# Performance work log

Measured on AMD Instinct MI355X. Metric: run time of the kernel, lower is better.

The kernel has to match this reference:

```python
import jax, jax.numpy as jnp
import numpy as np

C_DIM = 768
NH = 12
MLP_HIDDEN = 3072


def _ln(x, g, b, eps=1e-5):
    mu = x.mean(-1, keepdims=True)
    var = ((x - mu) ** 2).mean(-1, keepdims=True)
    return (x - mu) / jnp.sqrt(var + eps) * g + b


def _mha(x, Wqkv, nh, scale):
    # x: [N, L, C]; Wqkv: [C, 3C] packed as (3, nh, hd) on output dim
    N, L, C = x.shape
    hd = C // nh
    qkv = (x @ Wqkv).reshape(N, L, 3, nh, hd)
    q, k, v = qkv[:, :, 0], qkv[:, :, 1], qkv[:, :, 2]  # [N, L, nh, hd]
    a = jnp.einsum('nqhd,nkhd->nhqk', q, k) * scale
    a = jax.nn.softmax(a, axis=-1)
    o = jnp.einsum('nhqk,nkhd->nqhd', a, v).reshape(N, L, C)
    return o


def setup_inputs() -> dict:
    key = jax.random.key(0)
    ks = jax.random.split(key, 16)
    B, T, K, C = 4, 16, 196, C_DIM
    s = 0.02
    inp = {
        'x': jax.random.normal(ks[0], (B, 1 + K * T, C), jnp.float32),
        'B': B, 'T': T, 'K': K,
        'ln1_g': jnp.ones((C,)), 'ln1_b': jnp.zeros((C,)),
        'lnt_g': jnp.ones((C,)), 'lnt_b': jnp.zeros((C,)),
        'ln2_g': jnp.ones((C,)), 'ln2_b': jnp.zeros((C,)),
        'lncls_g': jnp.ones((C,)), 'lncls_b': jnp.zeros((C,)),
        'Wqkv_s': jax.random.normal(ks[1], (C, 3 * C)) * s,
        'Wproj_s': jax.random.normal(ks[2], (C, C)) * s,
        'bproj_s': jnp.zeros((C,)),
        'Wqkv4': jax.random.normal(ks[3], (C, 3 * C)) * s,
        'Wqkv8': jax.random.normal(ks[4], (C, 3 * C)) * s,
        'Wqkv16': jax.random.normal(ks[5], (C, 3 * C)) * s,
        'Wp4': jax.random.normal(ks[6], (C, C)) * s, 'bp4': jnp.zeros((C,)),
        'Wp8': jax.random.normal(ks[7], (C, C)) * s, 'bp8': jnp.zeros((C,)),
        'Wp16': jax.random.normal(ks[8], (C, C)) * s, 'bp16': jnp.zeros((C,)),
        'Wtfc': jax.random.normal(ks[9], (C, C)) * s, 'btfc': jnp.zeros((C,)),
        'Wfc1': jax.random.normal(ks[10], (C, MLP_HIDDEN)) * s, 'bfc1': jnp.zeros((MLP_HIDDEN,)),
        'Wfc2': jax.random.normal(ks[11], (MLP_HIDDEN, C)) * s, 'bfc2': jnp.zeros((C,)),
    }
    return inp


def reference(x, B, T, K, ln1_g, ln1_b, lnt_g, lnt_b, ln2_g, ln2_b,
              lncls_g, lncls_b, Wqkv_s, Wproj_s, bproj_s,
              Wqkv4, Wqkv8, Wqkv16, Wp4, bp4, Wp8, bp8, Wp16, bp16,
              Wtfc, btfc, Wfc1, bfc1, Wfc2, bfc2):
    C = x.shape[-1]
    nh = NH
    scale = (C // nh) ** -0.5
    t1, t2 = T // 4, T // 2

    # ---- multi-scale temporal attention (eval mode: all dropout identity) ----
    xt = x[:, 1:, :].reshape(B, K, T, C).reshape(B * K, T, C)
    xt_n = _ln(xt, lnt_g, lnt_b)
    x4 = _mha(xt_n[:, T - t1:], Wqkv4, nh, scale) @ Wp4 + bp4    # [BK, t1, C]
    x8 = _mha(xt_n[:, t2:], Wqkv8, nh, scale) @ Wp8 + bp8        # [BK, t2, C]
    x16 = _mha(xt_n, Wqkv16, nh, scale) @ Wp16 + bp16            # [BK, T, C]
    # windowed fusion of overlapping scales
    x8 = jnp.concatenate([x8[:, :t1], 0.5 * x8[:, t1:] + 0.5 * x4], axis=1)
    x16 = jnp.concatenate([x16[:, :t2], 0.5 * x16[:, t2:] + 0.5 * x8], axis=1)
    res_temp = x16.reshape(B, K * T, C)
    xt_full = res_temp @ Wtfc + btfc + x[:, 1:, :]               # [B, K*T, C]

    # ---- spatial attention with replicated CLS token ----
    init_cls = x[:, 0:1, :]                                      # [B, 1, C]
    cls_rep = jnp.broadcast_to(init_cls, (B, T, C)).reshape(B * T, 1, C)
    xs = xt_full.reshape(B, K, T, C).transpose(0, 2, 1, 3).reshape(B * T, K, C)
    xs = jnp.concatenate([cls_rep, xs], axis=1)                  # [B*T, K+1, C]
    res_spatial = _mha(_ln(xs, ln1_g, ln1_b), Wqkv_s, nh, scale) @ Wproj_s + bproj_s

    # ---- CLS aggregation over time ----
    cls_sp = _ln(res_spatial[:, 0, :].reshape(B, T, C), lncls_g, lncls_b)
    target = cls_sp[:, -1:, :]                                   # [B, 1, C]
    attn2 = jax.nn.softmax(jnp.einsum('bqc,btc->bqt', target, cls_sp), axis=-1)
    cls_sp = attn2 @ cls_sp                                      # [B, 1, C]

    x_s = res_spatial[:, 1:, :].reshape(B, T, K, C).transpose(0, 2, 1, 3).reshape(B, K * T, C)
    x_cat = jnp.concatenate([init_cls, xt_full], axis=1) + jnp.concatenate([cls_sp, x_s], axis=1)

    # ---- MLP residual ----
    h = _ln(x_cat, ln2_g, ln2_b)
    h = jax.nn.gelu(h @ Wfc1 + bfc1, approximate=False) @ Wfc2 + bfc2
    return x_cat + h
```

## Files before the change

### kernel.cpp

```cpp
#include <hip/hip_runtime.h>
#include <hip/hip_bf16.h>
#include <stdint.h>

#define BF16 __hip_bfloat16

typedef __attribute__((ext_vector_type(8))) short short8;
typedef __attribute__((ext_vector_type(2))) short short2v;
typedef __attribute__((ext_vector_type(4))) float floatx4;

typedef const __attribute__((address_space(1))) void* gas_cvp;
typedef __attribute__((address_space(3))) void* las_vp;

__device__ __forceinline__ float bf2f(BF16 v) { return __bfloat162float(v); }
__device__ __forceinline__ BF16 f2bf(float v) { return __float2bfloat16(v); }

__global__ __launch_bounds__(256) void wtrans(const float* __restrict__ W,
                                              BF16* __restrict__ Wt, int K, int N) {
    __shared__ float t[32][33];
    int k0 = blockIdx.x * 32, n0 = blockIdx.y * 32;
    int tx = threadIdx.x & 31, ty = threadIdx.x >> 5;
#pragma unroll
    for (int i = 0; i < 32; i += 8) t[ty + i][tx] = W[(size_t)(k0 + ty + i) * N + n0 + tx];
    __syncthreads();
#pragma unroll
    for (int i = 0; i < 32; i += 8)
        Wt[(size_t)(n0 + ty + i) * K + k0 + tx] = f2bf(t[tx][ty + i]);
}

struct WTJob { const float* src; BF16* dst; int K; int N; int boff; };
struct WTParams { WTJob j[12]; };

__global__ __launch_bounds__(256) void wtrans_all(WTParams P) {
    __shared__ float t[32][33];
    const int bid = blockIdx.x;
    int ji = 0;
#pragma unroll
    for (int i = 1; i < 12; ++i)
        if (bid >= P.j[i].boff) ji = i;
    const float* __restrict__ W = P.j[ji].src;
    BF16* __restrict__ Wt = P.j[ji].dst;
    const int K = P.j[ji].K, N = P.j[ji].N;
    const int lb = bid - P.j[ji].boff;
    const int kb = K >> 5;
    const int k0 = (lb % kb) * 32, n0 = (lb / kb) * 32;
    const int tx = threadIdx.x & 31, ty = threadIdx.x >> 5;
#pragma unroll
    for (int i = 0; i < 32; i += 8) t[ty + i][tx] = W[(size_t)(k0 + ty + i) * N + n0 + tx];
    __syncthreads();
#pragma unroll
    for (int i = 0; i < 32; i += 8)
        Wt[(size_t)(n0 + ty + i) * K + k0 + tx] = f2bf(t[tx][ty + i]);
}

template <int MODE>
__global__ __launch_bounds__(256) void ln_kernel(const float* __restrict__ src0,
                                                 const float* __restrict__ src1,
                                                 const BF16* __restrict__ srcb,
                                                 const float* __restrict__ g,
                                                 const float* __restrict__ bta,
                                                 BF16* __restrict__ dst_bf,
                                                 float* __restrict__ dst_f) {
    const int r = blockIdx.x, tid = threadIdx.x;
    float x0, x1, x2;
    {
        const float* src;
        if (MODE == 0) {
            int b = r / 3136, rr = r - b * 3136;
            src = src0 + ((size_t)b * 3137 + 1 + rr) * 768;
        } else if (MODE == 1) {
            int bt = r / 197, j = r - bt * 197;
            int b = bt >> 4, t = bt & 15;
            if (j == 0) src = src0 + (size_t)b * 3137 * 768;
            else        src = src1 + ((size_t)(b * 3137 + 1) + (size_t)(j - 1) * 16 + t) * 768;
        } else {
            src = src0 + (size_t)r * 768;
        }
        x0 = src[tid]; x1 = src[tid + 256]; x2 = src[tid + 512];
    }
    float s = x0 + x1 + x2;
    float ss = x0 * x0 + x1 * x1 + x2 * x2;
    __shared__ float red[8];
#pragma unroll
    for (int o = 32; o > 0; o >>= 1) { s += __shfl_down(s, o); ss += __shfl_down(ss, o); }
    if ((tid & 63) == 0) { red[tid >> 6] = s; red[4 + (tid >> 6)] = ss; }
    __syncthreads();
    s = red[0] + red[1] + red[2] + red[3];
    ss = red[4] + red[5] + red[6] + red[7];
    const float mu = s * (1.0f / 768.0f);
    const float var = ss * (1.0f / 768.0f) - mu * mu;
    const float rstd = rsqrtf(var + 1e-5f);
#pragma unroll
    for (int i = 0; i < 3; ++i) {
        int c = tid + i * 256;
        float xv = (i == 0) ? x0 : (i == 1) ? x1 : x2;
        float y = (xv - mu) * rstd * g[c] + bta[c];
        dst_bf[(size_t)r * 768 + c] = f2bf(y);
    }
}

template <int AMAP, int OMODE>
__device__ __forceinline__ void gemm_body(BF16* Al, BF16* Bl,
                                          int orig, int nwg, int gx,
                                          const BF16* __restrict__ A,
                                          const BF16* __restrict__ Bt,
                                          const float* __restrict__ bias,
                                          const void* res, void* Cout,
                                          int M, int N, int K) {
    const int tid = threadIdx.x;
    const int lane = tid & 63;
    const int w = tid >> 6;

    const int xcd = orig & 7;
    const int idx = orig >> 3;
    const int q8 = nwg >> 3, r8 = nwg & 7;
    const int wgid = (xcd < r8 ? xcd * (q8 + 1) : r8 * (q8 + 1) + (xcd - r8) * q8) + idx;
    const int bn0 = (wgid % gx) * 128;
    const int bm0 = (wgid / gx) * 128;

    const BF16* gsrc[8];
    BF16* ldst[8];
    const int rin = lane >> 3;
    const int kblk = (lane & 7) ^ rin;
#pragma unroll
    for (int j = 0; j < 8; ++j) {
        int c = w * 8 + j;
        if (c < 16) {
            int gr = bm0 + c * 8 + rin;
            if (gr > M - 1) gr = M - 1;
            if (AMAP == 1) gr = (gr >> 3) * 16 + 8 + (gr & 7);
            if (AMAP == 2) gr = (gr >> 2) * 16 + 12 + (gr & 3);
            gsrc[j] = A + (size_t)gr * K + kblk * 8;
            ldst[j] = Al + c * 512;
        } else {
            int gn = bn0 + (c - 16) * 8 + rin;
            gsrc[j] = Bt + (size_t)gn * K + kblk * 8;
            ldst[j] = Bl + (c - 16) * 512;
        }
    }

    const int wm = (w & 1) * 64;
    const int wn = (w >> 1) * 64;
    const int fr = lane & 15;
    const int fq = lane >> 4;
    const int sw = fr & 7;
    const int o0 = (fq ^ sw) * 8;
    const int o1 = ((fq + 4) ^ sw) * 8;
    const BF16* pa[4];
    const BF16* pb[4];
#pragma unroll
    for (int t = 0; t < 4; ++t) {
        pa[t] = Al + (wm + t * 16 + fr) * 64;
        pb[t] = Bl + (wn + t * 16 + fr) * 64;
    }

    floatx4 acc[4][4];
#pragma unroll
    for (int i = 0; i < 4; ++i)
#pragma unroll
        for (int j = 0; j < 4; ++j) acc[i][j] = (floatx4){0.f, 0.f, 0.f, 0.f};

    for (int k0 = 0; k0 < K; k0 += 64) {
#pragma unroll
        for (int j = 0; j < 8; ++j) {
            __builtin_amdgcn_global_load_lds((gas_cvp)gsrc[j], (las_vp)ldst[j], 16, 0, 0);
            gsrc[j] += 64;
        }
        __syncthreads();
        {
            short8 af[4], bfr[4];
#pragma unroll
            for (int t = 0; t < 4; ++t) {
                af[t] = *(const short8*)(pa[t] + o0);
                bfr[t] = *(const short8*)(pb[t] + o0);
            }
#pragma unroll
            for (int mt = 0; mt < 4; ++mt)
#pragma unroll
                for (int nt = 0; nt < 4; ++nt)
                    acc[mt][nt] = __builtin_amdgcn_mfma_f32_16x16x32_bf16(af[mt], bfr[nt], acc[mt][nt], 0, 0, 0);
#pragma unroll
            for (int t = 0; t < 4; ++t) {
                af[t] = *(const short8*)(pa[t] + o1);
                bfr[t] = *(const short8*)(pb[t] + o1);
            }
#pragma unroll
            for (int mt = 0; mt < 4; ++mt)
#pragma unroll
                for (int nt = 0; nt < 4; ++nt)
                    acc[mt][nt] = __builtin_amdgcn_mfma_f32_16x16x32_bf16(af[mt], bfr[nt], acc[mt][nt], 0, 0, 0);
        }
        __syncthreads();
    }

#pragma unroll
    for (int mt = 0; mt < 4; ++mt) {
#pragma unroll
        for (int nt = 0; nt < 4; ++nt) {
            const int gcol = bn0 + wn + nt * 16 + fr;
#pragma unroll
            for (int r = 0; r < 4; ++r) {
                const int grow = bm0 + wm + mt * 16 + fq * 4 + r;
                if (grow < M) {
                    float v = acc[mt][nt][r];
                    if (OMODE != 0 && OMODE != 8) v += bias[gcol];
                    if (OMODE == 0 || OMODE == 1) {
                        ((BF16*)Cout)[(size_t)grow * N + gcol] = f2bf(v);
                    } else if (OMODE == 2) {
                        int t8 = grow & 7;
                        int rr = (grow >> 3) * 16 + 8 + t8;
                        float w8 = (t8 < 4) ? 0.5f : 0.25f;
                        BF16* R = (BF16*)Cout;
                        size_t o = (size_t)rr * 768 + gcol;
                        R[o] = f2bf(0.5f * bf2f(R[o]) + w8 * v);
                    } else if (OMODE == 3) {
                        int t4 = grow & 3;
                        int rr = (grow >> 2) * 16 + 12 + t4;
                        BF16* R = (BF16*)Cout;
                        size_t o = (size_t)rr * 768 + gcol;
                        R[o] = f2bf(bf2f(R[o]) + 0.25f * v);
                    } else if (OMODE == 4) {
                        int b = grow / 3136;
                        size_t xrow = (size_t)b * 3137 + 1 + (grow - b * 3136);
                        ((float*)Cout)[xrow * 768 + gcol] =
                            v + ((const float*)res)[xrow * 768 + gcol];
                    } else if (OMODE == 6) {
                        float u = v * (0.7978845608f + 0.0356774081f * v * v);
                        v = v / (1.0f + __expf(-2.0f * u));
                        ((BF16*)Cout)[(size_t)grow * N + gcol] = f2bf(v);
                    } else {
                        v += ((const float*)res)[(size_t)grow * N + gcol];
                        ((float*)Cout)[(size_t)grow * N + gcol] = v;
                    }
                }
            }
        }
    }
}

template <int AMAP, int OMODE>
__global__ __launch_bounds__(256) void gemm_bf16(const BF16* __restrict__ A,
                                                 const BF16* __restrict__ Bt,
                                                 const float* __restrict__ bias,
                                                 const void* res,
                                                 void* Cout,
                                                 int M, int N, int K) {
    __shared__ BF16 Al[128 * 64];
    __shared__ BF16 Bl[128 * 64];
    const int gx = gridDim.x;
    const int nwg = gx * (int)gridDim.y;
    const int orig = (int)blockIdx.y * gx + (int)blockIdx.x;
    gemm_body<AMAP, OMODE>(Al, Bl, orig, nwg, gx, A, Bt, bias, res, Cout, M, N, K);
}

template <int AMAP0, int OMODE0, int AMAP1, int OMODE1>
__global__ __launch_bounds__(256) void gemm_dual(
        int nblk0, int gx0,
        const BF16* A0, const BF16* B0, const float* b0, const void* r0, void* C0,
        int M0, int N0, int K0,
        int gx1,
        const BF16* A1, const BF16* B1, const float* b1, const void* r1, void* C1,
        int M1, int N1, int K1) {
    __shared__ BF16 Al[128 * 64];
    __shared__ BF16 Bl[128 * 64];
    const int bid = blockIdx.x;
    if (bid < nblk0)
        gemm_body<AMAP0, OMODE0>(Al, Bl, bid, nblk0, gx0, A0, B0, b0, r0, C0, M0, N0, K0);
    else
        gemm_body<AMAP1, OMODE1>(Al, Bl, bid - nblk0, (int)gridDim.x - nblk0, gx1,
                                 A1, B1, b1, r1, C1, M1, N1, K1);
}

template <int L, int NT>
__global__ __launch_bounds__(NT) void temporal_attn(const BF16* __restrict__ qkv,
                                                    BF16* __restrict__ outp) {
    __shared__ float q[L * 64];
    __shared__ float k[L * 65];
    __shared__ float v[L * 64];
    __shared__ float S[L * L];
    const int bh = blockIdx.x;
    const int b = bh / 12, h = bh % 12;
    const int tid = threadIdx.x;
    const size_t rb = (size_t)b * L;
    for (int idx = tid; idx < L * 8; idx += NT) {
        int i = idx >> 3, d8 = (idx & 7) * 8;
        size_t base = (rb + i) * 2304 + h * 64 + d8;
        short8 qv = *(const short8*)(qkv + base);
        short8 kv = *(const short8*)(qkv + base + 768);
        short8 vv = *(const short8*)(qkv + base + 1536);
#pragma unroll
        for (int e = 0; e < 8; ++e) {
            q[i * 64 + d8 + e] = bf2f(((const BF16*)&qv)[e]);
            k[i * 65 + d8 + e] = bf2f(((const BF16*)&kv)[e]);
            v[i * 64 + d8 + e] = bf2f(((const BF16*)&vv)[e]);
        }
    }
    __syncthreads();
    for (int idx = tid; idx < L * L; idx += NT) {
        int i = idx / L, j = idx % L;
        float a = 0.f;
#pragma unroll
        for (int d = 0; d < 64; ++d) a += q[i * 64 + d] * k[j * 65 + d];
        S[idx] = a * 0.125f;
    }
    __syncthreads();
    if (tid < L) {
        float mx = -1e30f;
        for (int j = 0; j < L; ++j) mx = fmaxf(mx, S[tid * L + j]);
        float sm = 0.f;
        for (int j = 0; j < L; ++j) { float e = __expf(S[tid * L + j] - mx); S[tid * L + j] = e; sm += e; }
        float inv = 1.0f / sm;
        for (int j = 0; j < L; ++j) S[tid * L + j] *= inv;
    }
    __syncthreads();
    for (int idx = tid; idx < L * 8; idx += NT) {
        int i = idx >> 3, d8 = (idx & 7) * 8;
        float acc[8];
#pragma unroll
        for (int e = 0; e < 8; ++e) acc[e] = 0.f;
#pragma unroll
        for (int j = 0; j < L; ++j) {
            float sv = S[i * L + j];
#pragma unroll
            for (int e = 0; e < 8; ++e) acc[e] += sv * v[j * 64 + d8 + e];
        }
        short8 ov;
#pragma unroll
        for (int e = 0; e < 8; ++e) ((BF16*)&ov)[e] = f2bf(acc[e]);
        *(short8*)(outp + (rb + i) * 768 + h * 64 + d8) = ov;
    }
}

__global__ __launch_bounds__(256) void spatial_attn_mfma(const BF16* __restrict__ qkv,
                                                         BF16* __restrict__ outp) {
    const int bid = blockIdx.x;
    const int qt = bid & 3;
    const int h = (bid >> 2) % 12;
    const int bt = bid / 48;
    const int rowbase = bt * 197;
    __shared__ BF16 KsPl[208 * 72];
    __shared__ BF16 Vt[64 * 232];
    const int tid = threadIdx.x;
    const int lane = tid & 63;
    const int w = tid >> 6;
    const int ln = lane & 15;
    const int quad = lane >> 4;

    for (int it = tid; it < 208 * 8; it += 256) {
        int key = it >> 3, c = it & 7;
        int kc = key < 197 ? key : 196;
        short8 gk = *(const short8*)(qkv + (size_t)(rowbase + kc) * 2304 + 768 + h * 64 + c * 8);
        *(short8*)&KsPl[key * 72 + c * 8] = gk;
    }
    for (int it = tid; it < 112 * 8; it += 256) {
        int p = it >> 3, c = it & 7;
        int kc0 = (2 * p < 197) ? 2 * p : 196;
        int kc1 = (2 * p + 1 < 197) ? 2 * p + 1 : 196;
        short8 a = *(const short8*)(qkv + (size_t)(rowbase + kc0) * 2304 + 1536 + h * 64 + c * 8);
        short8 b = *(const short8*)(qkv + (size_t)(rowbase + kc1) * 2304 + 1536 + h * 64 + c * 8);
#pragma unroll
        for (int e = 0; e < 8; ++e) {
            short2v pr;
            pr[0] = a[e];
            pr[1] = b[e];
            *(short2v*)&Vt[(c * 8 + e) * 232 + 2 * p] = pr;
        }
    }
    __syncthreads();

    const int m0 = qt * 64 + w * 16;
    int qrow = m0 + ln; if (qrow > 196) qrow = 196;
    const BF16* qptr = qkv + (size_t)(rowbase + qrow) * 2304 + h * 64 + quad * 8;
    short8 aq0 = *(const short8*)(qptr);
    short8 aq1 = *(const short8*)(qptr + 32);

    floatx4 sacc[13];
#pragma unroll
    for (int nt = 0; nt < 13; ++nt) sacc[nt] = (floatx4){0.f, 0.f, 0.f, 0.f};
#pragma unroll
    for (int nt = 0; nt < 13; ++nt) {
        const BF16* kb = &KsPl[(nt * 16 + ln) * 72 + quad * 8];
        short8 b0 = *(const short8*)kb;
        short8 b1 = *(const short8*)(kb + 32);
        sacc[nt] = __builtin_amdgcn_mfma_f32_16x16x32_bf16(aq0, b0, sacc[nt], 0, 0, 0);
        sacc[nt] = __builtin_amdgcn_mfma_f32_16x16x32_bf16(aq1, b1, sacc[nt], 0, 0, 0);
    }
    __syncthreads();

#pragma unroll
    for (int r = 0; r < 4; ++r) {
        float mx = -1e30f;
#pragma unroll
        for (int nt = 0; nt < 13; ++nt) {
            float s = sacc[nt][r] * 0.125f;
            sacc[nt][r] = s;
            if (nt * 16 + ln < 197) mx = fmaxf(mx, s);
        }
        mx = fmaxf(mx, __shfl_xor(mx, 1));
        mx = fmaxf(mx, __shfl_xor(mx, 2));
        mx = fmaxf(mx, __shfl_xor(mx, 4));
        mx = fmaxf(mx, __shfl_xor(mx, 8));
        float sum = 0.f;
#pragma unroll
        for (int nt = 0; nt < 13; ++nt) {
            float e = (nt * 16 + ln < 197) ? __expf(sacc[nt][r] - mx) : 0.f;
            sacc[nt][r] = e;
            sum += e;
        }
        sum += __shfl_xor(sum, 1);
        sum += __shfl_xor(sum, 2);
        sum += __shfl_xor(sum, 4);
        sum += __shfl_xor(sum, 8);
        float inv = 1.0f / sum;
#pragma unroll
        for (int nt = 0; nt < 13; ++nt) sacc[nt][r] *= inv;
    }

    BF16* pw = KsPl + w * (16 * 232);
#pragma unroll
    for (int nt = 0; nt < 13; ++nt)
#pragma unroll
        for (int r = 0; r < 4; ++r)
            pw[(quad * 4 + r) * 232 + nt * 16 + ln] = f2bf(sacc[nt][r]);
#pragma unroll
    for (int r = 0; r < 4; ++r)
        pw[(quad * 4 + r) * 232 + 208 + ln] = f2bf(0.f);

    floatx4 oacc[4];
#pragma unroll
    for (int nt = 0; nt < 4; ++nt) oacc[nt] = (floatx4){0.f, 0.f, 0.f, 0.f};
    for (int kb = 0; kb < 7; ++kb) {
        short8 ap = *(const short8*)&pw[ln * 232 + kb * 32 + quad * 8];
#pragma unroll
        for (int nt = 0; nt < 4; ++nt) {
            short8 bv = *(const short8*)&Vt[(nt * 16 + ln) * 232 + kb * 32 + quad * 8];
            oacc[nt] = __builtin_amdgcn_mfma_f32_16x16x32_bf16(ap, bv, oacc[nt], 0, 0, 0);
        }
    }

#pragma unroll
    for (int nt = 0; nt < 4; ++nt) {
        int dim = nt * 16 + ln;
#pragma unroll
        for (int r = 0; r < 4; ++r) {
            int q = m0 + quad * 4 + r;
            if (q < 197)
                outp[(size_t)(rowbase + q) * 768 + h * 64 + dim] = f2bf(oacc[nt][r]);
        }
    }
}

__global__ __launch_bounds__(256) void cls_ln_attn_kernel(const BF16* __restrict__ res_sp,
                                                          const float* __restrict__ g,
                                                          const float* __restrict__ bta,
                                                          float* __restrict__ clsout) {
    const int b = blockIdx.x;
    const int tid = threadIdx.x;
    __shared__ float sLN[16][768];
    __shared__ float red[8];
    __shared__ float dots[16];
    __shared__ float aw[16];

    for (int t = 0; t < 16; ++t) {
        const BF16* src = res_sp + (size_t)((b * 16 + t) * 197) * 768;
        float x0 = bf2f(src[tid]);
        float x1 = bf2f(src[tid + 256]);
        float x2 = bf2f(src[tid + 512]);
        float s = x0 + x1 + x2;
        float ss = x0 * x0 + x1 * x1 + x2 * x2;
#pragma unroll
        for (int o = 32; o > 0; o >>= 1) { s += __shfl_down(s, o); ss += __shfl_down(ss, o); }
        if ((tid & 63) == 0) { red[tid >> 6] = s; red[4 + (tid >> 6)] = ss; }
        __syncthreads();
        s = red[0] + red[1] + red[2] + red[3];
        ss = red[4] + red[5] + red[6] + red[7];
        const float mu = s * (1.0f / 768.0f);
        const float var = ss * (1.0f / 768.0f) - mu * mu;
        const float rstd = rsqrtf(var + 1e-5f);
        sLN[t][tid]       = (x0 - mu) * rstd * g[tid] + bta[tid];
        sLN[t][tid + 256] = (x1 - mu) * rstd * g[tid + 256] + bta[tid + 256];
        sLN[t][tid + 512] = (x2 - mu) * rstd * g[tid + 512] + bta[tid + 512];
        __syncthreads();
    }

    const int t = tid >> 4, l16 = tid & 15;
    float p = 0.f;
    for (int c = l16; c < 768; c += 16) p += sLN[15][c] * sLN[t][c];
#pragma unroll
    for (int o = 8; o > 0; o >>= 1) p += __shfl_down(p, o, 16);
    if (l16 == 0) dots[t] = p;
    __syncthreads();
    if (tid == 0) {
        float mx = -1e30f;
        for (int j = 0; j < 16; ++j) mx = fmaxf(mx, dots[j]);
        float s = 0.f;
        for (int j = 0; j < 16; ++j) { aw[j] = __expf(dots[j] - mx); s += aw[j]; }
        float inv = 1.0f / s;
        for (int j = 0; j < 16; ++j) aw[j] *= inv;
    }
    __syncthreads();
    for (int c = tid; c < 768; c += 256) {
        float acc = 0.f;
#pragma unroll
        for (int j = 0; j < 16; ++j) acc += aw[j] * sLN[j][c];
        clsout[(size_t)b * 768 + c] = acc;
    }
}

__global__ __launch_bounds__(256) void xcat_ln_kernel(const float* __restrict__ x,
                                                      const BF16* __restrict__ res_sp,
                                                      const float* __restrict__ clsout,
                                                      const float* __restrict__ g,
                                                      const float* __restrict__ bta,
                                                      float* outbuf,
                                                      BF16* __restrict__ hln) {
    const int gidx = blockIdx.x;
    const int b = gidx / 3137, j = gidx - b * 3137;
    const int tid = threadIdx.x;
    float v0, v1, v2;
    if (j == 0) {
        const float* xr = x + (size_t)b * 3137 * 768;
        const float* cr = clsout + (size_t)b * 768;
        v0 = xr[tid] + cr[tid];
        v1 = xr[tid + 256] + cr[tid + 256];
        v2 = xr[tid + 512] + cr[tid + 512];
    } else {
        const int p = j - 1, k = p >> 4, t = p & 15;
        const BF16* rs = res_sp + (size_t)((b * 16 + t) * 197 + 1 + k) * 768;
        float* orow = outbuf + (size_t)gidx * 768;
        v0 = orow[tid] + bf2f(rs[tid]);
        v1 = orow[tid + 256] + bf2f(rs[tid + 256]);
        v2 = orow[tid + 512] + bf2f(rs[tid + 512]);
    }
    float* orow = outbuf + (size_t)gidx * 768;
    orow[tid] = v0; orow[tid + 256] = v1; orow[tid + 512] = v2;

    float s = v0 + v1 + v2;
    float ss = v0 * v0 + v1 * v1 + v2 * v2;
    __shared__ float red[8];
#pragma unroll
    for (int o = 32; o > 0; o >>= 1) { s += __shfl_down(s, o); ss += __shfl_down(ss, o); }
    if ((tid & 63) == 0) { red[tid >> 6] = s; red[4 + (tid >> 6)] = ss; }
    __syncthreads();
    s = red[0] + red[1] + red[2] + red[3];
    ss = red[4] + red[5] + red[6] + red[7];
    const float mu = s * (1.0f / 768.0f);
    const float var = ss * (1.0f / 768.0f) - mu * mu;
    const float rstd = rsqrtf(var + 1e-5f);
#pragma unroll
    for (int i = 0; i < 3; ++i) {
        int c = tid + i * 256;
        float xv = (i == 0) ? v0 : (i == 1) ? v1 : v2;
        hln[(size_t)gidx * 768 + c] = f2bf((xv - mu) * rstd * g[c] + bta[c]);
    }
}

extern "C" void kernel_launch(void* const* d_in, const int* in_sizes, int n_in,
                              void* d_out, int out_size, void* d_ws, size_t ws_size,
                              hipStream_t stream) {
    const float* x       = (const float*)d_in[0];
    const float* ln1_g   = (const float*)d_in[4];
    const float* ln1_b   = (const float*)d_in[5];
    const float* lnt_g   = (const float*)d_in[6];
    const float* lnt_b   = (const float*)d_in[7];
    const float* ln2_g   = (const float*)d_in[8];
    const float* ln2_b   = (const float*)d_in[9];
    const float* lncls_g = (const float*)d_in[10];
    const float* lncls_b = (const float*)d_in[11];
    const float* Wqkv_s  = (const float*)d_in[12];
    const float* Wproj_s = (const float*)d_in[13];
    const float* bproj_s = (const float*)d_in[14];
    const float* Wqkv4   = (const float*)d_in[15];
    const float* Wqkv8   = (const float*)d_in[16];
    const float* Wqkv16  = (const float*)d_in[17];
    const float* Wp4     = (const float*)d_in[18];
    const float* bp4     = (const float*)d_in[19];
    const float* Wp8     = (const float*)d_in[20];
    const float* bp8     = (const float*)d_in[21];
    const float* Wp16    = (const float*)d_in[22];
    const float* bp16    = (const float*)d_in[23];
    const float* Wtfc    = (const float*)d_in[24];
    const float* btfc    = (const float*)d_in[25];
    const float* Wfc1    = (const float*)d_in[26];
    const float* bfc1    = (const float*)d_in[27];
    const float* Wfc2    = (const float*)d_in[28];
    const float* bfc2    = (const float*)d_in[29];
    float* out = (float*)d_out;

    const size_t oW0 = 0;
    const size_t oW1 = 4718592;
    const size_t oR1 = 9437184;
    const size_t oR2 = 28803072;
    const size_t oR3 = 48070656;
    const size_t oR4 = 77119488;
    const size_t oCO = 96681984;
    const size_t NEED = 96694272;
    const size_t NEED_BIG = NEED + 29491200;
    const size_t NEED_C   = NEED_BIG + 38547456;
    if (ws_size < NEED) return;
    char* ws = (char*)d_ws;

    BF16* w0       = (BF16*)(ws + oW0);
    BF16* w1       = (BF16*)(ws + oW1);
    BF16* xtn      = (BF16*)(ws + oR1);
    BF16* atts     = (BF16*)(ws + oR1);
    BF16* hln      = (BF16*)(ws + oR1);
    BF16* res_temp = (BF16*)(ws + oR2);
    BF16* h1       = (BF16*)(ws + oR2);
    BF16* qkv      = (BF16*)(ws + oR3);
    BF16* att      = (BF16*)(ws + oR4);
    BF16* xsn      = (BF16*)(ws + oR4);
    BF16* res_sp   = (BF16*)(ws + oR4);
    float* clsout  = (float*)(ws + oCO);

    const bool big = (ws_size >= NEED_BIG);
    const bool featC = (ws_size >= NEED_C);
    BF16* h1b = featC ? (BF16*)(ws + NEED_BIG) : nullptr;
    BF16 *tqkv16, *tqkv8, *tqkv4, *tqkvs, *tp16, *tp8, *tp4, *ttfc, *tproj, *tfc1, *tfc2;
    if (big) {
        char* wx = ws + NEED;
        tqkv16 = (BF16*)wx; wx += 3538944;
        tqkv8  = (BF16*)wx; wx += 3538944;
        tqkv4  = (BF16*)wx; wx += 3538944;
        tqkvs  = (BF16*)wx; wx += 3538944;
        tp16   = (BF16*)wx; wx += 1179648;
        tp8    = (BF16*)wx; wx += 1179648;
        tp4    = (BF16*)wx; wx += 1179648;
        ttfc   = (BF16*)wx; wx += 1179648;
        tproj  = (BF16*)wx; wx += 1179648;
        tfc1   = (BF16*)wx; wx += 4718592;
        tfc2   = (BF16*)wx; wx += 4718592;
        WTParams P;
        P.j[0]  = { Wqkv16,                     tqkv16,                     768, 2304,     0 };
        P.j[1]  = { Wqkv8,                      tqkv8,                      768, 2304,  1728 };
        P.j[2]  = { Wqkv4,                      tqkv4,                      768, 2304,  3456 };
        P.j[3]  = { Wqkv_s,                     tqkvs,                      768, 2304,  5184 };
        P.j[4]  = { Wp16,                       tp16,                       768,  768,  6912 };
        P.j[5]  = { Wp8,                        tp8,                        768,  768,  7488 };
        P.j[6]  = { Wp4,                        tp4,                        768,  768,  8064 };
        P.j[7]  = { Wtfc,                       ttfc,                       768,  768,  8640 };
        P.j[8]  = { Wproj_s,                    tproj,                      768,  768,  9216 };
        P.j[9]  = { Wfc1,                       tfc1,                       768, 3072,  9792 };
        P.j[10] = { Wfc2,                       tfc2,                      1536,  768, 12096 };
        P.j[11] = { Wfc2 + (size_t)1536 * 768,  tfc2 + (size_t)768 * 1536, 1536,  768, 13248 };
        wtrans_all<<<14400, 256, 0, stream>>>(P);
    } else {
        tqkv16 = w0; tqkv8 = w0; tqkv4 = w0; tqkvs = w1;
        tp16 = w1; tp8 = w1; tp4 = w1; ttfc = w0; tproj = w0;
        tfc1 = w0; tfc2 = w1;
    }

    ln_kernel<0><<<12544, 256, 0, stream>>>(x, nullptr, nullptr, lnt_g, lnt_b, xtn, nullptr);

    if (!big) wtrans<<<dim3(24, 72), 256, 0, stream>>>(Wqkv16, tqkv16, 768, 2304);
    for (int c = 0; c < 2; ++c) {
        gemm_bf16<0, 0><<<dim3(18, 49), 256, 0, stream>>>(xtn + (size_t)c * 6272 * 768, tqkv16, nullptr, nullptr, qkv, 6272, 2304, 768);
        temporal_attn<16, 256><<<4704, 256, 0, stream>>>(qkv, att + (size_t)c * 6272 * 768);
    }

    if (!big) {
        wtrans<<<dim3(24, 24), 256, 0, stream>>>(Wp16, tp16, 768, 768);
        wtrans<<<dim3(24, 72), 256, 0, stream>>>(Wqkv8, tqkv8, 768, 2304);
    }
    gemm_dual<0, 1, 1, 0><<<588 + 882, 256, 0, stream>>>(
        588, 6, att, tp16, bp16, nullptr, res_temp, 12544, 768, 768,
        18, xtn, tqkv8, nullptr, nullptr, qkv, 6272, 2304, 768);
    temporal_attn<8, 64><<<9408, 64, 0, stream>>>(qkv, att);

    if (!big) {
        wtrans<<<dim3(24, 24), 256, 0, stream>>>(Wp8, tp8, 768, 768);
        wtrans<<<dim3(24, 72), 256, 0, stream>>>(Wqkv4, tqkv4, 768, 2304);
    }
    gemm_dual<0, 2, 2, 0><<<294 + 450, 256, 0, stream>>>(
        294, 6, att, tp8, bp8, nullptr, res_temp, 6272, 768, 768,
        18, xtn, tqkv4, nullptr, nullptr, qkv, 3136, 2304, 768);
    temporal_attn<4, 64><<<9408, 64, 0, stream>>>(qkv, att);

    if (!big) wtrans<<<dim3(24, 24), 256, 0, stream>>>(Wp4, tp4, 768, 768);
    gemm_bf16<0, 3><<<dim3(6, 25), 256, 0, stream>>>(att, tp4, bp4, nullptr, res_temp, 3136, 768, 768);

    if (!big) wtrans<<<dim3(24, 24), 256, 0, stream>>>(Wtfc, ttfc, 768, 768);
    gemm_bf16<0, 4><<<dim3(6, 98), 256, 0, stream>>>(res_temp, ttfc, btfc, x, out, 12544, 768, 768);

    ln_kernel<1><<<12608, 256, 0, stream>>>(x, out, nullptr, ln1_g, ln1_b, xsn, nullptr);
    if (!big) wtrans<<<dim3(24, 72), 256, 0, stream>>>(Wqkv_s, tqkvs, 768, 2304);
    for (int c = 0; c < 2; ++c) {
        gemm_bf16<0, 0><<<dim3(18, 50), 256, 0, stream>>>(xsn + (size_t)c * 6304 * 768, tqkvs, nullptr, nullptr, qkv, 6304, 2304, 768);
        spatial_attn_mfma<<<1536, 256, 0, stream>>>(qkv, atts + (size_t)c * 6304 * 768);
    }
    if (!big) wtrans<<<dim3(24, 24), 256, 0, stream>>>(Wproj_s, tproj, 768, 768);
    gemm_bf16<0, 1><<<dim3(6, 99), 256, 0, stream>>>(atts, tproj, bproj_s, nullptr, res_sp, 12608, 768, 768);

    cls_ln_attn_kernel<<<4, 256, 0, stream>>>(res_sp, lncls_g, lncls_b, clsout);

    xcat_ln_kernel<<<12548, 256, 0, stream>>>(x, res_sp, clsout, ln2_g, ln2_b, out, hln);

    if (!big) {
        wtrans<<<dim3(24, 96), 256, 0, stream>>>(Wfc1, tfc1, 768, 3072);
        wtrans<<<dim3(48, 24), 256, 0, stream>>>(Wfc2, tfc2, 1536, 768);
        wtrans<<<dim3(48, 24), 256, 0, stream>>>(Wfc2 + (size_t)1536 * 768, tfc2 + (size_t)768 * 1536, 1536, 768);
    }

    if (featC) {
        gemm_bf16<0, 6><<<dim3(12, 99), 256, 0, stream>>>(hln, tfc1, bfc1, nullptr, h1, 12548, 1536, 768);
        gemm_dual<0, 7, 0, 6><<<594 + 1188, 256, 0, stream>>>(
            594, 6, h1, tfc2, bfc2, out, out, 12548, 768, 1536,
            12, hln, tfc1 + (size_t)1536 * 768, bfc1 + 1536, nullptr, h1b, 12548, 1536, 768);
        gemm_bf16<0, 8><<<dim3(6, 99), 256, 0, stream>>>(h1b, tfc2 + (size_t)768 * 1536, nullptr, out, out, 12548, 768, 1536);
    } else {
        gemm_bf16<0, 6><<<dim3(12, 99), 256, 0, stream>>>(hln, tfc1, bfc1, nullptr, h1, 12548, 1536, 768);
        gemm_bf16<0, 7><<<dim3(6, 99), 256, 0, stream>>>(h1, tfc2, bfc2, out, out, 12548, 768, 1536);
        gemm_bf16<0, 6><<<dim3(12, 99), 256, 0, stream>>>(hln, tfc1 + (size_t)1536 * 768, bfc1 + 1536, nullptr, h1, 12548, 1536, 768);
        gemm_bf16<0, 8><<<dim3(6, 99), 256, 0, stream>>>(h1, tfc2 + (size_t)768 * 1536, nullptr, out, out, 12548, 768, 1536);
    }
}
```

Measured before the change: 926.7 us.

## Merge chunked QKV GEMMs and attention launches into paired dual-grid kernels

When the workspace is large enough, the two-chunk loops for temporal (L=16) and spatial QKV projection plus attention are replaced by single launches. A gemm_dual covers both chunks, writing into a second QKV buffer, and a paired attention kernel dispatches on block index. This cuts the launch count and gives each launch a larger grid, which should reduce tail effects and serialization between chunks. It costs extra workspace for the second QKV buffer, which aliases the h1b region used later.

```diff
diff --git a/kernel.cpp b/kernel.cpp
--- a/kernel.cpp
+++ b/kernel.cpp
@@ -271,13 +271,9 @@
 }
 
 template <int L, int NT>
-__global__ __launch_bounds__(NT) void temporal_attn(const BF16* __restrict__ qkv,
-                                                    BF16* __restrict__ outp) {
-    __shared__ float q[L * 64];
-    __shared__ float k[L * 65];
-    __shared__ float v[L * 64];
-    __shared__ float S[L * L];
-    const int bh = blockIdx.x;
+__device__ __forceinline__ void temporal_attn_body(float* q, float* k, float* v, float* S,
+                                                   const BF16* __restrict__ qkv,
+                                                   BF16* __restrict__ outp, int bh) {
     const int b = bh / 12, h = bh % 12;
     const int tid = threadIdx.x;
     const size_t rb = (size_t)b * L;
@@ -330,15 +326,36 @@
     }
 }
 
-__global__ __launch_bounds__(256) void spatial_attn_mfma(const BF16* __restrict__ qkv,
-                                                         BF16* __restrict__ outp) {
-    const int bid = blockIdx.x;
+template <int L, int NT>
+__global__ __launch_bounds__(NT) void temporal_attn(const BF16* __restrict__ qkv,
+                                                    BF16* __restrict__ outp) {
+    __shared__ float q[L * 64];
+    __shared__ float k[L * 65];
+    __shared__ float v[L * 64];
+    __shared__ float S[L * L];
+    temporal_attn_body<L, NT>(q, k, v, S, qkv, outp, blockIdx.x);
+}
+
+__global__ __launch_bounds__(256) void temporal_attn16_pair(const BF16* __restrict__ q0,
+                                                            BF16* __restrict__ o0,
+                                                            const BF16* __restrict__ q1,
+                                                            BF16* __restrict__ o1) {
+    __shared__ float q[16 * 64];
+    __shared__ float k[16 * 65];
+    __shared__ float v[16 * 64];
+    __shared__ float S[16 * 16];
+    const int bh = blockIdx.x;
+    if (bh < 4704) temporal_attn_body<16, 256>(q, k, v, S, q0, o0, bh);
+    else           temporal_attn_body<16, 256>(q, k, v, S, q1, o1, bh - 4704);
+}
+
+__device__ __forceinline__ void spatial_attn_body(BF16* KsPl, BF16* Vt,
+                                                  const BF16* __restrict__ qkv,
+                                                  BF16* __restrict__ outp, int bid) {
     const int qt = bid & 3;
     const int h = (bid >> 2) % 12;
     const int bt = bid / 48;
     const int rowbase = bt * 197;
-    __shared__ BF16 KsPl[208 * 72];
-    __shared__ BF16 Vt[64 * 232];
     const int tid = threadIdx.x;
     const int lane = tid & 63;
     const int w = tid >> 6;
@@ -447,6 +464,24 @@
                 outp[(size_t)(rowbase + q) * 768 + h * 64 + dim] = f2bf(oacc[nt][r]);
         }
     }
+}
+
+__global__ __launch_bounds__(256) void spatial_attn_mfma(const BF16* __restrict__ qkv,
+                                                         BF16* __restrict__ outp) {
+    __shared__ BF16 KsPl[208 * 72];
+    __shared__ BF16 Vt[64 * 232];
+    spatial_attn_body(KsPl, Vt, qkv, outp, blockIdx.x);
+}
+
+__global__ __launch_bounds__(256) void spatial_attn_pair(const BF16* __restrict__ q0,
+                                                         BF16* __restrict__ o0,
+                                                         const BF16* __restrict__ q1,
+                                                         BF16* __restrict__ o1) {
+    __shared__ BF16 KsPl[208 * 72];
+    __shared__ BF16 Vt[64 * 232];
+    const int bid = blockIdx.x;
+    if (bid < 1536) spatial_attn_body(KsPl, Vt, q0, o0, bid);
+    else            spatial_attn_body(KsPl, Vt, q1, o1, bid - 1536);
 }
 
 __global__ __launch_bounds__(256) void cls_ln_attn_kernel(const BF16* __restrict__ res_sp,
@@ -614,7 +649,8 @@
 
     const bool big = (ws_size >= NEED_BIG);
     const bool featC = (ws_size >= NEED_C);
-    BF16* h1b = featC ? (BF16*)(ws + NEED_BIG) : nullptr;
+    BF16* h1b  = featC ? (BF16*)(ws + NEED_BIG) : nullptr;
+    BF16* qkv2 = featC ? (BF16*)(ws + NEED_BIG) : nullptr;
     BF16 *tqkv16, *tqkv8, *tqkv4, *tqkvs, *tp16, *tp8, *tp4, *ttfc, *tproj, *tfc1, *tfc2;
     if (big) {
         char* wx = ws + NEED;
@@ -652,9 +688,16 @@
     ln_kernel<0><<<12544, 256, 0, stream>>>(x, nullptr, nullptr, lnt_g, lnt_b, xtn, nullptr);
 
     if (!big) wtrans<<<dim3(24, 72), 256, 0, stream>>>(Wqkv16, tqkv16, 768, 2304);
-    for (int c = 0; c < 2; ++c) {
-        gemm_bf16<0, 0><<<dim3(18, 49), 256, 0, stream>>>(xtn + (size_t)c * 6272 * 768, tqkv16, nullptr, nullptr, qkv, 6272, 2304, 768);
-        temporal_attn<16, 256><<<4704, 256, 0, stream>>>(qkv, att + (size_t)c * 6272 * 768);
+    if (featC) {
+        gemm_dual<0, 0, 0, 0><<<882 + 882, 256, 0, stream>>>(
+            882, 18, xtn, tqkv16, nullptr, nullptr, qkv, 6272, 2304, 768,
+            18, xtn + (size_t)6272 * 768, tqkv16, nullptr, nullptr, qkv2, 6272, 2304, 768);
+        temporal_attn16_pair<<<9408, 256, 0, stream>>>(qkv, att, qkv2, att + (size_t)6272 * 768);
+    } else {
+        for (int c = 0; c < 2; ++c) {
+            gemm_bf16<0, 0><<<dim3(18, 49), 256, 0, stream>>>(xtn + (size_t)c * 6272 * 768, tqkv16, nullptr, nullptr, qkv, 6272, 2304, 768);
+            temporal_attn<16, 256><<<4704, 256, 0, stream>>>(qkv, att + (size_t)c * 6272 * 768);
+        }
     }
 
     if (!big) {
@@ -683,9 +726,16 @@
 
     ln_kernel<1><<<12608, 256, 0, stream>>>(x, out, nullptr, ln1_g, ln1_b, xsn, nullptr);
     if (!big) wtrans<<<dim3(24, 72), 256, 0, stream>>>(Wqkv_s, tqkvs, 768, 2304);
-    for (int c = 0; c < 2; ++c) {
-        gemm_bf16<0, 0><<<dim3(18, 50), 256, 0, stream>>>(xsn + (size_t)c * 6304 * 768, tqkvs, nullptr, nullptr, qkv, 6304, 2304, 768);
-        spatial_attn_mfma<<<1536, 256, 0, stream>>>(qkv, atts + (size_t)c * 6304 * 768);
+    if (featC) {
+        gemm_dual<0, 0, 0, 0><<<900 + 900, 256, 0, stream>>>(
+            900, 18, xsn, tqkvs, nullptr, nullptr, qkv, 6304, 2304, 768,
+            18, xsn + (size_t)6304 * 768, tqkvs, nullptr, nullptr, qkv2, 6304, 2304, 768);
+        spatial_attn_pair<<<3072, 256, 0, stream>>>(qkv, atts, qkv2, atts + (size_t)6304 * 768);
+    } else {
+        for (int c = 0; c < 2; ++c) {
+            gemm_bf16<0, 0><<<dim3(18, 50), 256, 0, stream>>>(xsn + (size_t)c * 6304 * 768, tqkvs, nullptr, nullptr, qkv, 6304, 2304, 768);
+            spatial_attn_mfma<<<1536, 256, 0, stream>>>(qkv, atts + (size_t)c * 6304 * 768);
+        }
     }
     if (!big) wtrans<<<dim3(24, 24), 256, 0, stream>>>(Wproj_s, tproj, 768, 768);
     gemm_bf16<0, 1><<<dim3(6, 99), 256, 0, stream>>>(atts, tproj, bproj_s, nullptr, res_sp, 12608, 768, 768);
```

Result: slower. 1.041 ms (+12.3%).
